# Kernel optimization log

Hardware: AMD Instinct MI355X
Metric: run time of the kernel (lower is better)

The kernel has to match this reference:

```python
import jax, jax.numpy as jnp
import numpy as np

N_NODES = 50000
N_EDGES = 1600000
F_IN = 256
HID = 256
HEADS = 8
HD = HID // HEADS  # 32
SLOPE = 0.2
EPS = 1e-5


def setup_inputs() -> dict:
    key = jax.random.key(0)
    ks = jax.random.split(key, 10)
    node_features = jax.random.normal(ks[0], (N_NODES, F_IN), jnp.float32)
    edge_index = jax.random.randint(ks[1], (2, N_EDGES), 0, N_NODES, jnp.int32)
    s = 1.0 / np.sqrt(F_IN)
    W = jax.random.uniform(ks[2], (HEADS, F_IN, HD), jnp.float32, -s, s)
    bw = jax.random.uniform(ks[3], (HEADS, HD), jnp.float32, -s, s)
    sa = 1.0 / np.sqrt(2 * HD)
    A = jax.random.uniform(ks[4], (HEADS, 2 * HD), jnp.float32, -sa, sa)
    ba = jax.random.uniform(ks[5], (HEADS,), jnp.float32, -sa, sa)
    gamma = jnp.ones((HEADS, HD), jnp.float32)
    beta = jnp.zeros((HEADS, HD), jnp.float32)
    so = 1.0 / np.sqrt(HD)
    Wout = jax.random.uniform(ks[6], (HD, HID), jnp.float32, -so, so)
    bout = jax.random.uniform(ks[7], (HID,), jnp.float32, -so, so)
    return dict(node_features=node_features, edge_index=edge_index, W=W, bw=bw,
                A=A, ba=ba, gamma=gamma, beta=beta, Wout=Wout, bout=bout)


def _head(x, W, bw, a, ba, gamma, beta, tgt, src):
    h = x @ W + bw                         # [N, d]
    # attn(concat(h_i, h_j)) = h_i @ a1 + h_j @ a2 + ba  (linear over concat)
    si = h @ a[:HD]                        # [N]
    sj = h @ a[HD:]                        # [N]
    e = si[tgt] + sj[src] + ba             # [E]
    e = jnp.where(e >= 0, e, SLOPE * e)    # leaky_relu
    # scatter_softmax over edges grouped by target node (stable)
    m = jax.ops.segment_max(e, tgt, num_segments=N_NODES)
    ex = jnp.exp(e - m[tgt])
    den = jax.ops.segment_sum(ex, tgt, num_segments=N_NODES)
    alpha = ex / den[tgt]                  # [E]  (dropout in eval mode = identity)
    msg = alpha[:, None] * h[src]          # [E, d]
    agg = jax.ops.segment_sum(msg, tgt, num_segments=N_NODES)  # [N, d]
    out = agg + h                          # skip connection
    out = jnp.where(out > 0, out, jnp.expm1(out))  # ELU
    mu = out.mean(axis=-1, keepdims=True)
    var = out.var(axis=-1, keepdims=True)
    return (out - mu) * jax.lax.rsqrt(var + EPS) * gamma + beta


def reference(node_features, edge_index, W, bw, A, ba, gamma, beta, Wout, bout):
    tgt = edge_index[0]
    src = edge_index[1]
    heads = jax.vmap(_head, in_axes=(None, 0, 0, 0, 0, 0, 0, None, None))(
        node_features, W, bw, A, ba, gamma, beta, tgt, src)   # [H, N, d]
    mean = heads.mean(axis=0)                                  # [N, d]
    y = mean @ Wout + bout                                     # [N, HID]
    return jnp.where(y > 0, y, jnp.expm1(y))                   # ELU
```

## Files before the change

### kernel.cpp

```cpp
#include <hip/hip_runtime.h>
#include <hip/hip_bf16.h>
#include <hip/hip_fp16.h>

#define N_NODES 50000
#define N_EDGES 1600000
#define HEADS 8
#define HD 32
#define FIN 256
#define HID 256

typedef unsigned short u16;
typedef unsigned int u32;

typedef short s8v __attribute__((ext_vector_type(8)));
typedef float f4v __attribute__((ext_vector_type(4)));
typedef float fx4 __attribute__((ext_vector_type(4)));

__device__ __forceinline__ u32 pk2(float lo, float hi) {
  __hip_bfloat162 b = __float22bfloat162_rn(make_float2(lo, hi));
  union { __hip_bfloat162 b2; u32 u; } c;
  c.b2 = b;
  return c.u;
}

__global__ __launch_bounds__(512) void k_gemm(
    const float* __restrict__ X, const float* __restrict__ W,
    const float* __restrict__ bw, const float* __restrict__ A,
    __half* __restrict__ Hb, float* __restrict__ si, float* __restrict__ sj) {
  __shared__ __align__(16) u16 Xs[128 * 40];
  __shared__ __align__(16) u16 Wt[256 * 40];

  const int t = threadIdx.x;
  const int m0 = blockIdx.x * 128;
  const int w = t >> 6;
  const int lane = t & 63;
  const int l15 = lane & 15;
  const int quad = lane >> 4;
  const int wm = (w >> 2) * 64;
  const int wn = (w & 3) * 64;

  f4v acc[4][4];
#pragma unroll
  for (int i = 0; i < 4; i++)
#pragma unroll
    for (int j = 0; j < 4; j++) acc[i][j] = (f4v){0.f, 0.f, 0.f, 0.f};

  const int nl = t & 255;
  const int half = t >> 8;
  const int gh = nl >> 5, gd = nl & 31;

  for (int k0 = 0; k0 < FIN; k0 += 32) {
#pragma unroll
    for (int p = 0; p < 2; p++) {
      int row = p * 64 + (t >> 3);
      int f4 = t & 7;
      int node = m0 + row;
      fx4 xv = (fx4){0.f, 0.f, 0.f, 0.f};
      if (node < N_NODES)
        xv = __builtin_nontemporal_load((const fx4*)&X[node * FIN + k0 + f4 * 4]);
      u32* dst = (u32*)&Xs[row * 40 + f4 * 4];
      dst[0] = pk2(xv[0], xv[1]);
      dst[1] = pk2(xv[2], xv[3]);
    }
    {
      const float* wp = W + gh * (FIN * HD) + (k0 + half * 16) * HD + gd;
#pragma unroll
      for (int j = 0; j < 8; j++) {
        float lo = wp[(2 * j) * HD];
        float hi = wp[(2 * j + 1) * HD];
        *(u32*)&Wt[nl * 40 + half * 16 + 2 * j] = pk2(lo, hi);
      }
    }
    __syncthreads();
    s8v af[4], bf[4];
#pragma unroll
    for (int mi = 0; mi < 4; mi++)
      af[mi] = *(const s8v*)&Xs[(wm + mi * 16 + l15) * 40 + quad * 8];
#pragma unroll
    for (int ni = 0; ni < 4; ni++)
      bf[ni] = *(const s8v*)&Wt[(wn + ni * 16 + l15) * 40 + quad * 8];
#pragma unroll
    for (int mi = 0; mi < 4; mi++)
#pragma unroll
      for (int ni = 0; ni < 4; ni++)
        acc[mi][ni] = __builtin_amdgcn_mfma_f32_16x16x32_bf16(af[mi], bf[ni], acc[mi][ni], 0, 0, 0);
    __syncthreads();
  }

  const int head0 = wn >> 5;
  const int head1 = head0 + 1;
  float c1a0 = A[head0 * 64 + l15],      c1a1 = A[head0 * 64 + 16 + l15];
  float c2a0 = A[head0 * 64 + 32 + l15], c2a1 = A[head0 * 64 + 48 + l15];
  float c1b0 = A[head1 * 64 + l15],      c1b1 = A[head1 * 64 + 16 + l15];
  float c2b0 = A[head1 * 64 + 32 + l15], c2b1 = A[head1 * 64 + 48 + l15];

#pragma unroll
  for (int mi = 0; mi < 4; mi++) {
#pragma unroll
    for (int ni = 0; ni < 4; ni++) {
      float b = bw[wn + ni * 16 + l15];
#pragma unroll
      for (int r = 0; r < 4; r++) acc[mi][ni][r] += b;
    }
    const int rbase = m0 + wm + mi * 16 + quad * 4;
#pragma unroll
    for (int r = 0; r < 4; r++) {
      int node = rbase + r;
      if (node < N_NODES) {
#pragma unroll
        for (int ni = 0; ni < 4; ni++) {
          int col = wn + ni * 16 + l15;
          Hb[node * HID + col] = __float2half_rn(acc[mi][ni][r]);
        }
      }
    }
    float s1a[4], s2a[4], s1b[4], s2b[4];
#pragma unroll
    for (int r = 0; r < 4; r++) {
      s1a[r] = acc[mi][0][r] * c1a0 + acc[mi][1][r] * c1a1;
      s2a[r] = acc[mi][0][r] * c2a0 + acc[mi][1][r] * c2a1;
      s1b[r] = acc[mi][2][r] * c1b0 + acc[mi][3][r] * c1b1;
      s2b[r] = acc[mi][2][r] * c2b0 + acc[mi][3][r] * c2b1;
    }
#pragma unroll
    for (int off = 1; off <= 8; off <<= 1) {
#pragma unroll
      for (int r = 0; r < 4; r++) {
        s1a[r] += __shfl_xor(s1a[r], off);
        s2a[r] += __shfl_xor(s2a[r], off);
        s1b[r] += __shfl_xor(s1b[r], off);
        s2b[r] += __shfl_xor(s2b[r], off);
      }
    }
    if (l15 == 0) {
#pragma unroll
      for (int r = 0; r < 4; r++) {
        int node = rbase + r;
        if (node < N_NODES) {
          si[node * HEADS + head0] = s1a[r];
          sj[node * HEADS + head0] = s2a[r];
          si[node * HEADS + head1] = s1b[r];
          sj[node * HEADS + head1] = s2b[r];
        }
      }
    }
  }
}

__global__ void k_hist(const int* __restrict__ tgt, int* __restrict__ cnt) {
  int e = blockIdx.x * 256 + threadIdx.x;
  if (e < N_EDGES) atomicAdd(&cnt[tgt[e]], 1);
}

__global__ __launch_bounds__(256) void k_scan1(const int* __restrict__ cnt,
    int* __restrict__ excl, int* __restrict__ bsum) {
  __shared__ int s[256];
  const int t = threadIdx.x;
  const int i = blockIdx.x * 256 + t;
  int v = (i < N_NODES) ? cnt[i] : 0;
  s[t] = v;
  __syncthreads();
  int x = v;
  for (int off = 1; off < 256; off <<= 1) {
    int y = (t >= off) ? s[t - off] : 0;
    __syncthreads();
    x += y;
    s[t] = x;
    __syncthreads();
  }
  if (i < N_NODES) excl[i] = x - v;
  if (t == 255) bsum[blockIdx.x] = x;
}

__global__ __launch_bounds__(256) void k_scan2(const int* __restrict__ bsum,
                                               int* __restrict__ boff) {
  __shared__ int s[256];
  const int t = threadIdx.x;
  int v = (t < 196) ? bsum[t] : 0;
  s[t] = v;
  __syncthreads();
  int x = v;
  for (int off = 1; off < 256; off <<= 1) {
    int y = (t >= off) ? s[t - off] : 0;
    __syncthreads();
    x += y;
    s[t] = x;
    __syncthreads();
  }
  if (t < 196) boff[t] = x - v;
}

__global__ void k_scan3(const int* __restrict__ excl, const int* __restrict__ boff,
                        int* __restrict__ rowptr, int* __restrict__ cursor) {
  int i = blockIdx.x * 256 + threadIdx.x;
  if (i < N_NODES) {
    int v = excl[i] + boff[blockIdx.x];
    rowptr[i] = v;
    cursor[i] = v;
  }
}

__global__ void k_scatter(const int* __restrict__ tgt, const int* __restrict__ src,
                          int* __restrict__ cursor, int* __restrict__ sortedSrc) {
  int e = blockIdx.x * 256 + threadIdx.x;
  if (e < N_EDGES) {
    int tg = tgt[e];
    int pos = atomicAdd(&cursor[tg], 1);
    sortedSrc[pos] = src[e];
  }
}

__global__ __launch_bounds__(256) void k_fused(
    const __half* __restrict__ Hb, const float* __restrict__ si,
    const float* __restrict__ sj, const float* __restrict__ ba,
    const float* __restrict__ gamma, const float* __restrict__ beta,
    const float* __restrict__ Wout, const float* __restrict__ bout,
    const int* __restrict__ rowptr, const int* __restrict__ cnt,
    const int* __restrict__ sortedSrc, float* __restrict__ out) {
  const int t = threadIdx.x;
  const int lane = t & 63;
  const int n = blockIdx.x * 4 + (t >> 6);
  const int cg = lane & 31;
  const int es = lane >> 5;
  const int hh = cg >> 2;
  const int start = rowptr[n];
  const int deg = cnt[n];

  const float sb = si[n * HEADS + hh] + ba[hh];
  const char* hbBase = (const char*)Hb + 16 * cg;
  const int* ss = sortedSrc + start;

  float acc[8] = {0.f, 0.f, 0.f, 0.f, 0.f, 0.f, 0.f, 0.f};
  float den = 0.f;
#pragma unroll 4
  for (int slot = es; slot < deg; slot += 2) {
    int s = __builtin_nontemporal_load(ss + slot);
    float e = sb + sj[s * HEADS + hh];
    e = (e >= 0.f) ? e : 0.2f * e;
    float exv = __expf(e);
    float4 hb4 = *(const float4*)(hbBase + (size_t)s * (HID * 2));
    const __half2* hp = (const __half2*)&hb4;
#pragma unroll
    for (int d = 0; d < 4; d++) {
      acc[2 * d]     += exv * __low2float(hp[d]);
      acc[2 * d + 1] += exv * __high2float(hp[d]);
    }
    den += exv;
  }
#pragma unroll
  for (int j = 0; j < 8; j++) acc[j] += __shfl_xor(acc[j], 32);
  den += __shfl_xor(den, 32);

  float4 h4 = *(const float4*)((const char*)Hb + (size_t)n * (HID * 2) + 16 * cg);
  const __half2* hq = (const __half2*)&h4;
  float inv = (deg > 0) ? __fdividef(1.f, den) : 0.f;
  float v[8], sum = 0.f, sq = 0.f;
#pragma unroll
  for (int j = 0; j < 8; j++) {
    float hv = (j & 1) ? __high2float(hq[j >> 1]) : __low2float(hq[j >> 1]);
    float x = acc[j] * inv + hv;
    x = (x > 0.f) ? x : (__expf(x) - 1.f);
    v[j] = x;
    sum += x;
    sq += x * x;
  }
  sum += __shfl_xor(sum, 1); sq += __shfl_xor(sq, 1);
  sum += __shfl_xor(sum, 2); sq += __shfl_xor(sq, 2);
  float mu = sum * (1.f / 32.f);
  float var = sq * (1.f / 32.f) - mu * mu;
  float rstd = rsqrtf(var + 1e-5f);
  fx4 g0 = *(const fx4*)&gamma[cg * 8];
  fx4 g1 = *(const fx4*)&gamma[cg * 8 + 4];
  fx4 b0 = *(const fx4*)&beta[cg * 8];
  fx4 b1 = *(const fx4*)&beta[cg * 8 + 4];
  float m2[8];
#pragma unroll
  for (int j = 0; j < 8; j++) {
    float g = (j < 4) ? g0[j] : g1[j - 4];
    float bb = (j < 4) ? b0[j] : b1[j - 4];
    m2[j] = (v[j] - mu) * rstd * g + bb;
  }
#pragma unroll
  for (int j = 0; j < 8; j++) {
    m2[j] += __shfl_xor(m2[j], 4);
    m2[j] += __shfl_xor(m2[j], 8);
    m2[j] += __shfl_xor(m2[j], 16);
  }

  fx4 y = *(const fx4*)&bout[4 * lane];
#pragma unroll
  for (int q = 0; q < 4; q++) {
    float mv[8];
#pragma unroll
    for (int j = 0; j < 8; j++) mv[j] = __shfl(m2[j], q) * 0.125f;
#pragma unroll
    for (int j = 0; j < 8; j++) {
      fx4 w4 = *(const fx4*)&Wout[(q * 8 + j) * HID + 4 * lane];
      y += mv[j] * w4;
    }
  }
#pragma unroll
  for (int c = 0; c < 4; c++) y[c] = (y[c] > 0.f) ? y[c] : (__expf(y[c]) - 1.f);
  __builtin_nontemporal_store(y, (fx4*)&out[(size_t)n * HID + 4 * lane]);
}

extern "C" void kernel_launch(void* const* d_in, const int* in_sizes, int n_in,
                              void* d_out, int out_size, void* d_ws, size_t ws_size,
                              hipStream_t stream) {
  const float* X     = (const float*)d_in[0];
  const int*   EI    = (const int*)d_in[1];
  const float* W     = (const float*)d_in[2];
  const float* bw    = (const float*)d_in[3];
  const float* A     = (const float*)d_in[4];
  const float* ba    = (const float*)d_in[5];
  const float* gamma = (const float*)d_in[6];
  const float* beta  = (const float*)d_in[7];
  const float* Wout  = (const float*)d_in[8];
  const float* bout  = (const float*)d_in[9];
  float* out = (float*)d_out;
  const int* tgt = EI;
  const int* src = EI + N_EDGES;

  char* ws = (char*)d_ws;
  size_t off = 0;
  auto alloc = [&](size_t bytes) -> void* {
    void* p = ws + off;
    off += bytes;
    off = (off + 255) & ~(size_t)255;
    return p;
  };
  __half* Hb       = (__half*)alloc((size_t)N_NODES * HID * 2);
  float* si        = (float*)alloc((size_t)N_NODES * HEADS * 4);
  float* sj        = (float*)alloc((size_t)N_NODES * HEADS * 4);
  int*   cnt       = (int*)  alloc((size_t)N_NODES * 4);
  int*   excl      = (int*)  alloc((size_t)N_NODES * 4);
  int*   bsum      = (int*)  alloc(256 * 4);
  int*   boff      = (int*)  alloc(256 * 4);
  int*   rowptr    = (int*)  alloc((size_t)N_NODES * 4);
  int*   cursor    = (int*)  alloc((size_t)N_NODES * 4);
  int*   sortedSrc = (int*)  alloc((size_t)N_EDGES * 4);

  hipMemsetAsync(cnt, 0, (size_t)N_NODES * 4, stream);
  k_hist<<<(N_EDGES + 255) / 256, 256, 0, stream>>>(tgt, cnt);
  k_scan1<<<196, 256, 0, stream>>>(cnt, excl, bsum);
  k_scan2<<<1, 256, 0, stream>>>(bsum, boff);
  k_scan3<<<196, 256, 0, stream>>>(excl, boff, rowptr, cursor);
  k_scatter<<<(N_EDGES + 255) / 256, 256, 0, stream>>>(tgt, src, cursor, sortedSrc);
  k_gemm<<<(N_NODES + 127) / 128, 512, 0, stream>>>(X, W, bw, A, Hb, si, sj);
  k_fused<<<(N_NODES + 3) / 4, 256, 0, stream>>>(Hb, si, sj, ba, gamma, beta,
                                                 Wout, bout, rowptr, cnt,
                                                 sortedSrc, out);
}
```

Measured before the change: 495.9 us.

## Pre-transpose W to bf16 once and shrink GEMM tiles to 64 rows

Adds a small pre-pass kernel that converts W to bf16 in a column-major [col][k] layout, so the GEMM loads W tiles with vectorized 16-byte copies instead of strided scalar float loads plus per-block conversion. The GEMM block shrinks from 128 rows and 512 threads to 64 rows and 256 threads, giving more blocks for 50000 nodes. Each block now rereads the full W tile for half as many rows, and there is one extra kernel launch.

```diff
diff --git a/kernel.cpp b/kernel.cpp
--- a/kernel.cpp
+++ b/kernel.cpp
@@ -23,21 +23,29 @@
   return c.u;
 }
 
-__global__ __launch_bounds__(512) void k_gemm(
-    const float* __restrict__ X, const float* __restrict__ W,
+__global__ __launch_bounds__(256) void k_prepw(const float* __restrict__ W,
+                                               u16* __restrict__ Wp) {
+  int id = blockIdx.x * 256 + threadIdx.x;
+  int col = id >> 8;
+  int k = id & 255;
+  int h = col >> 5, d = col & 31;
+  Wp[col * 256 + k] = (u16)(pk2(W[h * 8192 + k * 32 + d], 0.f) & 0xFFFFu);
+}
+
+__global__ __launch_bounds__(256) void k_gemm(
+    const float* __restrict__ X, const u16* __restrict__ Wp,
     const float* __restrict__ bw, const float* __restrict__ A,
     __half* __restrict__ Hb, float* __restrict__ si, float* __restrict__ sj) {
-  __shared__ __align__(16) u16 Xs[128 * 40];
+  __shared__ __align__(16) u16 Xs[64 * 40];
   __shared__ __align__(16) u16 Wt[256 * 40];
 
   const int t = threadIdx.x;
-  const int m0 = blockIdx.x * 128;
+  const int m0 = blockIdx.x * 64;
   const int w = t >> 6;
   const int lane = t & 63;
   const int l15 = lane & 15;
   const int quad = lane >> 4;
-  const int wm = (w >> 2) * 64;
-  const int wn = (w & 3) * 64;
+  const int wn = w * 64;
 
   f4v acc[4][4];
 #pragma unroll
@@ -45,37 +53,35 @@
 #pragma unroll
     for (int j = 0; j < 4; j++) acc[i][j] = (f4v){0.f, 0.f, 0.f, 0.f};
 
-  const int nl = t & 255;
-  const int half = t >> 8;
-  const int gh = nl >> 5, gd = nl & 31;
+  const int srow = t >> 2;
+  const int spart = t & 3;
 
   for (int k0 = 0; k0 < FIN; k0 += 32) {
-#pragma unroll
-    for (int p = 0; p < 2; p++) {
-      int row = p * 64 + (t >> 3);
-      int f4 = t & 7;
-      int node = m0 + row;
-      fx4 xv = (fx4){0.f, 0.f, 0.f, 0.f};
-      if (node < N_NODES)
-        xv = __builtin_nontemporal_load((const fx4*)&X[node * FIN + k0 + f4 * 4]);
-      u32* dst = (u32*)&Xs[row * 40 + f4 * 4];
-      dst[0] = pk2(xv[0], xv[1]);
-      dst[1] = pk2(xv[2], xv[3]);
-    }
     {
-      const float* wp = W + gh * (FIN * HD) + (k0 + half * 16) * HD + gd;
-#pragma unroll
-      for (int j = 0; j < 8; j++) {
-        float lo = wp[(2 * j) * HD];
-        float hi = wp[(2 * j + 1) * HD];
-        *(u32*)&Wt[nl * 40 + half * 16 + 2 * j] = pk2(lo, hi);
+      int node = m0 + srow;
+      fx4 xa = (fx4){0.f, 0.f, 0.f, 0.f}, xb = xa;
+      if (node < N_NODES) {
+        const float* xp = &X[node * FIN + k0 + spart * 8];
+        xa = __builtin_nontemporal_load((const fx4*)xp);
+        xb = __builtin_nontemporal_load((const fx4*)(xp + 4));
       }
+      u32* dst = (u32*)&Xs[srow * 40 + spart * 8];
+      dst[0] = pk2(xa[0], xa[1]);
+      dst[1] = pk2(xa[2], xa[3]);
+      dst[2] = pk2(xb[0], xb[1]);
+      dst[3] = pk2(xb[2], xb[3]);
+    }
+#pragma unroll
+    for (int c2 = 0; c2 < 4; c2++) {
+      int cc = srow + c2 * 64;
+      *(fx4*)&Wt[cc * 40 + spart * 8] =
+          *(const fx4*)&Wp[cc * 256 + k0 + spart * 8];
     }
     __syncthreads();
     s8v af[4], bf[4];
 #pragma unroll
     for (int mi = 0; mi < 4; mi++)
-      af[mi] = *(const s8v*)&Xs[(wm + mi * 16 + l15) * 40 + quad * 8];
+      af[mi] = *(const s8v*)&Xs[(mi * 16 + l15) * 40 + quad * 8];
 #pragma unroll
     for (int ni = 0; ni < 4; ni++)
       bf[ni] = *(const s8v*)&Wt[(wn + ni * 16 + l15) * 40 + quad * 8];
@@ -102,7 +108,7 @@
 #pragma unroll
       for (int r = 0; r < 4; r++) acc[mi][ni][r] += b;
     }
-    const int rbase = m0 + wm + mi * 16 + quad * 4;
+    const int rbase = m0 + mi * 16 + quad * 4;
 #pragma unroll
     for (int r = 0; r < 4; r++) {
       int node = rbase + r;
@@ -286,7 +292,6 @@
     m2[j] += __shfl_xor(m2[j], 8);
     m2[j] += __shfl_xor(m2[j], 16);
   }
-
   fx4 y = *(const fx4*)&bout[4 * lane];
 #pragma unroll
   for (int q = 0; q < 4; q++) {
@@ -339,14 +344,16 @@
   int*   rowptr    = (int*)  alloc((size_t)N_NODES * 4);
   int*   cursor    = (int*)  alloc((size_t)N_NODES * 4);
   int*   sortedSrc = (int*)  alloc((size_t)N_EDGES * 4);
+  u16*   Wp        = (u16*)  alloc((size_t)HID * FIN * 2);
 
   hipMemsetAsync(cnt, 0, (size_t)N_NODES * 4, stream);
+  k_prepw<<<256, 256, 0, stream>>>(W, Wp);
   k_hist<<<(N_EDGES + 255) / 256, 256, 0, stream>>>(tgt, cnt);
   k_scan1<<<196, 256, 0, stream>>>(cnt, excl, bsum);
   k_scan2<<<1, 256, 0, stream>>>(bsum, boff);
   k_scan3<<<196, 256, 0, stream>>>(excl, boff, rowptr, cursor);
   k_scatter<<<(N_EDGES + 255) / 256, 256, 0, stream>>>(tgt, src, cursor, sortedSrc);
-  k_gemm<<<(N_NODES + 127) / 128, 512, 0, stream>>>(X, W, bw, A, Hb, si, sj);
+  k_gemm<<<(N_NODES + 63) / 64, 256, 0, stream>>>(X, Wp, bw, A, Hb, si, sj);
   k_fused<<<(N_NODES + 3) / 4, 256, 0, stream>>>(Hb, si, sj, ba, gamma, beta,
                                                  Wout, bout, rowptr, cnt,
                                                  sortedSrc, out);
```

New measurement: 506.4 us. +2.1%, slower.
